# Kernel optimization log

Hardware: AMD Instinct MI355X
Metric: run time of the kernel (lower is better)

## Reference

```python
import jax, jax.numpy as jnp
import numpy as np

B, S, HIDDEN = 2, 2048, 1024
NUM_HEADS, HEAD_DIM = 16, 64
STRIDE = 128
NEG = -10000.0


def _strided_mask(seq_len):
    # Sparse Transformer strided pattern: causal, local window of STRIDE,
    # plus every STRIDE-th previous position.
    i = jnp.arange(seq_len)[:, None]
    j = jnp.arange(seq_len)[None, :]
    diff = i - j
    allowed = (diff >= 0) & ((diff < STRIDE) | (diff % STRIDE == 0))
    return jnp.where(allowed, 0.0, NEG).astype(jnp.float32)  # [S, S]


def setup_inputs() -> dict:
    key = jax.random.key(0)
    k0, k1, k2, k3, k4 = jax.random.split(key, 5)
    hidden_states = jax.random.normal(k0, (B, S, HIDDEN), dtype=jnp.float32)
    attention_mask = jnp.zeros((B, 1, 1, S), dtype=jnp.float32)
    W_q = jax.random.normal(k1, (HIDDEN, HIDDEN), dtype=jnp.float32) * 0.02
    b_q = jnp.zeros((HIDDEN,), dtype=jnp.float32)
    W_v = jax.random.normal(k2, (HIDDEN, HIDDEN), dtype=jnp.float32) * 0.02
    b_v = jnp.zeros((HIDDEN,), dtype=jnp.float32)
    return {"hidden_states": hidden_states, "attention_mask": attention_mask,
            "W_q": W_q, "b_q": b_q, "W_v": W_v, "b_v": b_v}


def _heads(x):
    b, s, _ = x.shape
    return x.reshape(b, s, NUM_HEADS, HEAD_DIM).transpose(0, 2, 1, 3)  # [B,H,S,d]


def reference(hidden_states, attention_mask, W_q, b_q, W_v, b_v):
    q = _heads(hidden_states @ W_q + b_q)  # [B,H,S,d]
    v = _heads(hidden_states @ W_v + b_v)  # [B,H,S,d]
    hash_mask = _strided_mask(q.shape[-2])  # [S,S], broadcast over B,H
    # NB: source computes matmul(query, query^T) -- Q used for both sides.
    scores = jnp.einsum('bhid,bhjd->bhij', q, q) + hash_mask
    scores = scores / jnp.sqrt(jnp.asarray(HEAD_DIM, scores.dtype))
    scores = scores + attention_mask
    probs = jax.nn.softmax(scores, axis=-1)  # dropout p=0 (eval)
    ctx = jnp.einsum('bhij,bhjd->bhid', probs, v)  # [B,H,S,d]
    b = ctx.shape[0]
    return ctx.transpose(0, 2, 1, 3).reshape(b, -1, NUM_HEADS * HEAD_DIM)
```

## Files before the change

kernel.cpp:

```cpp
#include <hip/hip_runtime.h>

typedef __attribute__((ext_vector_type(8))) short short8;
typedef __attribute__((ext_vector_type(4))) float float4v;

__device__ inline float bf2f(ushort u) {
    unsigned v = ((unsigned)u) << 16;
    return __builtin_bit_cast(float, v);
}
__device__ inline ushort f2bf(float f) {
    unsigned u = __builtin_bit_cast(unsigned, f);
    u += 0x7FFFu + ((u >> 16) & 1u);
    return (ushort)(u >> 16);
}

__global__ __launch_bounds__(256) void transpose_w(
    const float* __restrict__ Wq, const float* __restrict__ Wv,
    ushort* __restrict__ Wtq, ushort* __restrict__ Wtv) {
    __shared__ ushort tile[64][68];
    const float* W = blockIdx.z ? Wv : Wq;
    ushort* Wt     = blockIdx.z ? Wtv : Wtq;
    const int k0 = blockIdx.y * 64, n0 = blockIdx.x * 64;
    const int tid = threadIdx.x;
    const int rr = tid >> 4;
    const int cc = (tid & 15) * 4;
    union U4 { ushort u[4]; uint2 v; };
#pragma unroll
    for (int i = 0; i < 4; ++i) {
        int row = rr + i * 16;
        float4v f = *(const float4v*)(W + (size_t)(k0 + row) * 1024 + n0 + cc);
        U4 x;
#pragma unroll
        for (int j = 0; j < 4; ++j) x.u[j] = f2bf(f[j]);
        *(uint2*)&tile[row][cc] = x.v;
    }
    __syncthreads();
#pragma unroll
    for (int i = 0; i < 4; ++i) {
        int row = rr + i * 16;
        U4 o;
#pragma unroll
        for (int j = 0; j < 4; ++j) o.u[j] = tile[cc + j][row];
        *(uint2*)(Wt + (size_t)(n0 + row) * 1024 + k0 + cc) = o.v;
    }
}

__global__ __launch_bounds__(256) void qv_gemm(
    const float* __restrict__ hs,
    const ushort* __restrict__ Wtq, const ushort* __restrict__ Wtv,
    const float* __restrict__ bq, const float* __restrict__ bv,
    ushort* __restrict__ q_ws, ushort* __restrict__ v_ws) {
    __shared__ ushort Al[128][72];
    __shared__ ushort Bl[128][72];
    const ushort* Wt  = blockIdx.z ? Wtv : Wtq;
    const float* bias = blockIdx.z ? bv : bq;
    ushort* out       = blockIdx.z ? v_ws : q_ws;
    const int m0 = blockIdx.y * 128;
    const int n0 = blockIdx.x * 128;
    const int tid = threadIdx.x;
    const int wid = tid >> 6, lane = tid & 63;
    const int quad = lane >> 4, l16 = lane & 15;
    const int wm = (wid >> 1) * 64, wn = (wid & 1) * 64;

    float4v acc[4][4] = {};

    for (int kt = 0; kt < 1024; kt += 64) {
        __syncthreads();
#pragma unroll
        for (int i = 0; i < 4; ++i) {
            int c = tid + i * 256;
            int row = c >> 3, col = (c & 7) * 8;
            const float* src = hs + (size_t)(m0 + row) * 1024 + kt + col;
            float4v f0 = *(const float4v*)(src);
            float4v f1 = *(const float4v*)(src + 4);
            union { ushort u[8]; uint4 v; } pk;
#pragma unroll
            for (int j = 0; j < 4; ++j) { pk.u[j] = f2bf(f0[j]); pk.u[4 + j] = f2bf(f1[j]); }
            *(uint4*)&Al[row][col] = pk.v;
            *(uint4*)&Bl[row][col] = *(const uint4*)(Wt + (size_t)(n0 + row) * 1024 + kt + col);
        }
        __syncthreads();
#pragma unroll
        for (int ks = 0; ks < 2; ++ks) {
            short8 af[4], bfr[4];
#pragma unroll
            for (int mt = 0; mt < 4; ++mt)
                af[mt] = *(const short8*)&Al[wm + mt * 16 + l16][ks * 32 + quad * 8];
#pragma unroll
            for (int nt = 0; nt < 4; ++nt)
                bfr[nt] = *(const short8*)&Bl[wn + nt * 16 + l16][ks * 32 + quad * 8];
#pragma unroll
            for (int mt = 0; mt < 4; ++mt)
#pragma unroll
                for (int nt = 0; nt < 4; ++nt)
                    acc[mt][nt] = __builtin_amdgcn_mfma_f32_16x16x32_bf16(
                        af[mt], bfr[nt], acc[mt][nt], 0, 0, 0);
        }
    }
#pragma unroll
    for (int mt = 0; mt < 4; ++mt) {
#pragma unroll
        for (int nt = 0; nt < 4; ++nt) {
            int coln = n0 + wn + nt * 16 + l16;
            float bsv = bias[coln];
            int hh = coln >> 6, dd = coln & 63;
#pragma unroll
            for (int reg = 0; reg < 4; ++reg) {
                int r = m0 + wm + mt * 16 + quad * 4 + reg;
                int bb = r >> 11, s = r & 2047;
                out[(((size_t)bb * 16 + hh) * 2048 + s) * 64 + dd] =
                    f2bf(acc[mt][nt][reg] + bsv);
            }
        }
    }
}

__global__ __launch_bounds__(512) void attn(
    const ushort* __restrict__ q_ws, const ushort* __restrict__ v_ws,
    const float* __restrict__ amask, float* __restrict__ out) {
    const int t = blockIdx.x, h = blockIdx.y, b = blockIdx.z;

    __shared__ ushort Kw[256][72];
    __shared__ ushort Vt[64][266];
    __shared__ ushort Pl[128][266];
    __shared__ float  Sstr[128][17];
    __shared__ float  am[2048];

    const int tid = threadIdx.x;
    const int wid = tid >> 6, lane = tid & 63;
    const int quad = lane >> 4, l16 = lane & 15;
    const int r0 = wid * 16;
    const size_t qbase = ((size_t)b * 16 + h) * 2048 * 64;
    const int base_row = (t - 1) * 128;
    const int nk = (t >= 2) ? (t - 1) : 0;

    *(float4v*)&am[tid * 4] = *(const float4v*)(amask + (size_t)b * 2048 + tid * 4);
#pragma unroll
    for (int i = 0; i < 4; ++i) {
        int c = tid + i * 512;
        int row = c >> 3, col = (c & 7) * 8;
        int jg = base_row + row; if (jg < 0) jg = 0;
        *(uint4*)&Kw[row][col] = *(const uint4*)(q_ws + qbase + (size_t)jg * 64 + col);
    }
    {
        int j = tid & 255, dh0 = (tid >> 8) * 32;
        int jg = base_row + j; if (jg < 0) jg = 0;
        const ushort* src = v_ws + qbase + (size_t)jg * 64 + dh0;
#pragma unroll
        for (int d = 0; d < 32; d += 8) {
            union { uint4 v; ushort u[8]; } tmp;
            tmp.v = *(const uint4*)(src + d);
#pragma unroll
            for (int jj = 0; jj < 8; ++jj) Vt[dh0 + d + jj][j] = tmp.u[jj];
        }
    }
    __syncthreads();

    float4v sacc[16] = {};
#pragma unroll
    for (int ks = 0; ks < 2; ++ks) {
        short8 af = *(const short8*)&Kw[128 + r0 + l16][ks * 32 + quad * 8];
#pragma unroll
        for (int nt = 0; nt < 16; ++nt) {
            short8 bfr = *(const short8*)&Kw[nt * 16 + l16][ks * 32 + quad * 8];
            sacc[nt] = __builtin_amdgcn_mfma_f32_16x16x32_bf16(af, bfr, sacc[nt], 0, 0, 0);
        }
    }

    const int sr = tid >> 2;
    const int dq = (tid & 3) * 16;
    if (nk > 0) {
        float qv[16];
#pragma unroll
        for (int d = 0; d < 16; d += 8) {
            union { uint4 v; ushort u[8]; } tmp;
            tmp.v = *(const uint4*)&Kw[128 + sr][dq + d];
#pragma unroll
            for (int j = 0; j < 8; ++j) qv[d + j] = bf2f(tmp.u[j]);
        }
        for (int k = 0; k < nk; ++k) {
            const ushort* kr = q_ws + qbase + (size_t)(k * 128 + sr) * 64 + dq;
            float p = 0.f;
#pragma unroll
            for (int d = 0; d < 16; d += 8) {
                union { uint4 v; ushort u[8]; } tmp;
                tmp.v = *(const uint4*)(kr + d);
#pragma unroll
                for (int jj = 0; jj < 8; ++jj) p += qv[d + jj] * bf2f(tmp.u[jj]);
            }
            p += __shfl_xor(p, 1);
            p += __shfl_xor(p, 2);
            if ((tid & 3) == 0)
                Sstr[sr][k] = p * 0.125f + am[k * 128 + sr];
        }
    }
    __syncthreads();

#pragma unroll
    for (int reg = 0; reg < 4; ++reg) {
        int rr = r0 + quad * 4 + reg;
        float sv[16];
#pragma unroll
        for (int nt = 0; nt < 16; ++nt) {
            int c = nt * 16 + l16;
            bool allowed = (c >= rr) && (c <= rr + 128) && (t > 0 || c >= 128);
            int ci = base_row + c; if (ci < 0) ci = 0;
            sv[nt] = allowed ? sacc[nt][reg] * 0.125f + am[ci] : -INFINITY;
        }
        float sstr_v = (l16 < nk) ? Sstr[rr][l16] : -INFINITY;
        float m = sstr_v;
#pragma unroll
        for (int nt = 0; nt < 16; ++nt) m = fmaxf(m, sv[nt]);
#pragma unroll
        for (int off = 1; off < 16; off <<= 1) m = fmaxf(m, __shfl_xor(m, off));

        float es = (l16 < nk) ? __expf(sstr_v - m) : 0.f;
        float sum = es;
#pragma unroll
        for (int nt = 0; nt < 16; ++nt) {
            float e = (sv[nt] == -INFINITY) ? 0.f : __expf(sv[nt] - m);
            sv[nt] = e; sum += e;
        }
#pragma unroll
        for (int off = 1; off < 16; off <<= 1) sum += __shfl_xor(sum, off);
        float rden = 1.f / sum;
#pragma unroll
        for (int nt = 0; nt < 16; ++nt)
            Pl[rr][nt * 16 + l16] = f2bf(sv[nt] * rden);
        if (l16 < nk)
            Sstr[rr][l16] = es * rden;
    }
    __syncthreads();

    float4v cacc[4] = {};
#pragma unroll
    for (int ks = 0; ks < 8; ++ks) {
        short8 af = *(const short8*)&Pl[r0 + l16][ks * 32 + quad * 8];
#pragma unroll
        for (int nt = 0; nt < 4; ++nt) {
            short8 bfr = *(const short8*)&Vt[nt * 16 + l16][ks * 32 + quad * 8];
            cacc[nt] = __builtin_amdgcn_mfma_f32_16x16x32_bf16(af, bfr, cacc[nt], 0, 0, 0);
        }
    }
    __syncthreads();

    float* ctxp = (float*)&Pl[0][0];
    {
        float acc16[16] = {};
        for (int k = 0; k < nk; ++k) {
            float p = Sstr[sr][k];
            const ushort* vr = v_ws + qbase + (size_t)(k * 128 + sr) * 64 + dq;
#pragma unroll
            for (int d = 0; d < 16; d += 8) {
                union { uint4 v; ushort u[8]; } tmp;
                tmp.v = *(const uint4*)(vr + d);
#pragma unroll
                for (int j = 0; j < 8; ++j) acc16[d + j] += p * bf2f(tmp.u[j]);
            }
        }
#pragma unroll
        for (int d = 0; d < 16; d += 4)
            *(float4v*)&ctxp[sr * 68 + dq + d] = *(const float4v*)&acc16[d];
    }
    __syncthreads();

    const size_t obase = ((size_t)b * 2048 + (size_t)t * 128) * 1024 + (size_t)h * 64;
#pragma unroll
    for (int nt = 0; nt < 4; ++nt)
#pragma unroll
        for (int reg = 0; reg < 4; ++reg) {
            int rr = r0 + quad * 4 + reg;
            int d = nt * 16 + l16;
            out[obase + (size_t)rr * 1024 + d] = cacc[nt][reg] + ctxp[rr * 68 + d];
        }
}

extern "C" void kernel_launch(void* const* d_in, const int* in_sizes, int n_in,
                              void* d_out, int out_size, void* d_ws, size_t ws_size,
                              hipStream_t stream) {
    int ihs = -1, iam = -1, iw1 = -1, iw2 = -1, ib1 = -1, ib2 = -1;
    for (int i = 0; i < n_in; ++i) {
        int s = in_sizes[i];
        if      (s == 4194304) { if (ihs < 0) ihs = i; }
        else if (s == 4096)    { if (iam < 0) iam = i; }
        else if (s == 1048576) { if (iw1 < 0) iw1 = i; else if (iw2 < 0) iw2 = i; }
        else if (s == 1024)    { if (ib1 < 0) ib1 = i; else if (ib2 < 0) ib2 = i; }
    }
    if (ihs < 0) ihs = 0; if (iam < 0) iam = 1;
    if (iw1 < 0) iw1 = 2; if (ib1 < 0) ib1 = 3;
    if (iw2 < 0) iw2 = 4; if (ib2 < 0) ib2 = 5;

    const float* hs    = (const float*)d_in[ihs];
    const float* amask = (const float*)d_in[iam];
    const float* Wq    = (const float*)d_in[iw1];
    const float* bq    = (const float*)d_in[ib1];
    const float* Wv    = (const float*)d_in[iw2];
    const float* bv    = (const float*)d_in[ib2];
    float* out = (float*)d_out;

    char* ws = (char*)d_ws;
    ushort* Wtq  = (ushort*)(ws);
    ushort* Wtv  = (ushort*)(ws + (1u << 21));
    ushort* q_ws = (ushort*)(ws + (2u << 21));
    ushort* v_ws = (ushort*)(ws + (2u << 21) + (1u << 23));

    transpose_w<<<dim3(16, 16, 2), 256, 0, stream>>>(Wq, Wv, Wtq, Wtv);
    qv_gemm<<<dim3(8, 32, 2), 256, 0, stream>>>(hs, Wtq, Wtv, bq, bv, q_ws, v_ws);
    attn<<<dim3(16, 16, 2), 512, 0, stream>>>(q_ws, v_ws, amask, out);
}
```

Baseline: 157.5 us.

## Pre-convert hidden states to bf16 and stage GEMM tiles via direct global-to-LDS loads

Adds a separate kernel that converts hidden_states to bf16 once, so the QV GEMM no longer converts fp32 to bf16 inside every tile load. The GEMM then fills its shared-memory tiles with global_load_lds direct copies into unpadded 64-wide rows. The attention grid is also remapped so that neighbouring blocks cover different heads with the same t. The costs are an extra launch plus a bf16 copy of the activations round-tripping through memory, and likely LDS bank conflicts now that row padding is gone.

```diff
diff --git a/kernel.cpp b/kernel.cpp
--- a/kernel.cpp
+++ b/kernel.cpp
@@ -11,6 +11,27 @@
     unsigned u = __builtin_bit_cast(unsigned, f);
     u += 0x7FFFu + ((u >> 16) & 1u);
     return (ushort)(u >> 16);
+}
+
+__device__ inline void gload_lds16(const ushort* g, ushort* l) {
+    __builtin_amdgcn_global_load_lds(
+        (const __attribute__((address_space(1))) unsigned int*)g,
+        (__attribute__((address_space(3))) unsigned int*)l,
+        16, 0, 0);
+}
+
+__global__ __launch_bounds__(256) void convert_hs(
+    const float* __restrict__ hs, ushort* __restrict__ hsb) {
+    const size_t base = ((size_t)blockIdx.x * 256 + threadIdx.x) * 16;
+    union { ushort u[16]; uint4 v[2]; } o;
+#pragma unroll
+    for (int q = 0; q < 4; ++q) {
+        float4v f = *(const float4v*)(hs + base + q * 4);
+#pragma unroll
+        for (int j = 0; j < 4; ++j) o.u[q * 4 + j] = f2bf(f[j]);
+    }
+    *(uint4*)(hsb + base)     = o.v[0];
+    *(uint4*)(hsb + base + 8) = o.v[1];
 }
 
 __global__ __launch_bounds__(256) void transpose_w(
@@ -45,38 +66,34 @@
 }
 
 __global__ __launch_bounds__(256) void qv_gemm(
-    const float* __restrict__ hs,
+    const ushort* __restrict__ hsb,
     const ushort* __restrict__ Wtq, const ushort* __restrict__ Wtv,
     const float* __restrict__ bq, const float* __restrict__ bv,
     ushort* __restrict__ q_ws, ushort* __restrict__ v_ws) {
-    __shared__ ushort Al[128][72];
-    __shared__ ushort Bl[128][72];
+    __shared__ ushort Al[128 * 64];
+    __shared__ ushort Bl[128 * 64];
     const ushort* Wt  = blockIdx.z ? Wtv : Wtq;
     const float* bias = blockIdx.z ? bv : bq;
     ushort* out       = blockIdx.z ? v_ws : q_ws;
-    const int m0 = blockIdx.y * 128;
-    const int n0 = blockIdx.x * 128;
+    const int m0 = blockIdx.y * 128, n0 = blockIdx.x * 128;
     const int tid = threadIdx.x;
     const int wid = tid >> 6, lane = tid & 63;
     const int quad = lane >> 4, l16 = lane & 15;
     const int wm = (wid >> 1) * 64, wn = (wid & 1) * 64;
+    const int rbase = 32 * wid;
+    const int srow = lane >> 3, scol = (lane & 7) * 8;
 
     float4v acc[4][4] = {};
 
     for (int kt = 0; kt < 1024; kt += 64) {
         __syncthreads();
 #pragma unroll
-        for (int i = 0; i < 4; ++i) {
-            int c = tid + i * 256;
-            int row = c >> 3, col = (c & 7) * 8;
-            const float* src = hs + (size_t)(m0 + row) * 1024 + kt + col;
-            float4v f0 = *(const float4v*)(src);
-            float4v f1 = *(const float4v*)(src + 4);
-            union { ushort u[8]; uint4 v; } pk;
-#pragma unroll
-            for (int j = 0; j < 4; ++j) { pk.u[j] = f2bf(f0[j]); pk.u[4 + j] = f2bf(f1[j]); }
-            *(uint4*)&Al[row][col] = pk.v;
-            *(uint4*)&Bl[row][col] = *(const uint4*)(Wt + (size_t)(n0 + row) * 1024 + kt + col);
+        for (int c8 = 0; c8 < 4; ++c8) {
+            int row = rbase + c8 * 8;
+            gload_lds16(hsb + (size_t)(m0 + row + srow) * 1024 + kt + scol,
+                        &Al[row * 64]);
+            gload_lds16(Wt + (size_t)(n0 + row + srow) * 1024 + kt + scol,
+                        &Bl[row * 64]);
         }
         __syncthreads();
 #pragma unroll
@@ -84,10 +101,10 @@
             short8 af[4], bfr[4];
 #pragma unroll
             for (int mt = 0; mt < 4; ++mt)
-                af[mt] = *(const short8*)&Al[wm + mt * 16 + l16][ks * 32 + quad * 8];
+                af[mt] = *(const short8*)&Al[(wm + mt * 16 + l16) * 64 + (ks * 4 + quad) * 8];
 #pragma unroll
             for (int nt = 0; nt < 4; ++nt)
-                bfr[nt] = *(const short8*)&Bl[wn + nt * 16 + l16][ks * 32 + quad * 8];
+                bfr[nt] = *(const short8*)&Bl[(wn + nt * 16 + l16) * 64 + (ks * 4 + quad) * 8];
 #pragma unroll
             for (int mt = 0; mt < 4; ++mt)
 #pragma unroll
@@ -117,7 +134,11 @@
 __global__ __launch_bounds__(512) void attn(
     const ushort* __restrict__ q_ws, const ushort* __restrict__ v_ws,
     const float* __restrict__ amask, float* __restrict__ out) {
-    const int t = blockIdx.x, h = blockIdx.y, b = blockIdx.z;
+    const int lin = blockIdx.x + 16 * blockIdx.y;
+    const int u8 = lin & 7, v32 = lin >> 3;
+    const int t = v32 & 15;
+    const int h = u8 + ((v32 >> 4) << 3);
+    const int b = blockIdx.z;
 
     __shared__ ushort Kw[256][72];
     __shared__ ushort Vt[64][266];
@@ -300,10 +321,12 @@
     char* ws = (char*)d_ws;
     ushort* Wtq  = (ushort*)(ws);
     ushort* Wtv  = (ushort*)(ws + (1u << 21));
-    ushort* q_ws = (ushort*)(ws + (2u << 21));
-    ushort* v_ws = (ushort*)(ws + (2u << 21) + (1u << 23));
-
+    ushort* hsb  = (ushort*)(ws + (2u << 21));
+    ushort* q_ws = (ushort*)(ws + (2u << 21) + (1u << 23));
+    ushort* v_ws = (ushort*)(ws + (2u << 21) + (2u << 23));
+
+    convert_hs<<<1024, 256, 0, stream>>>(hs, hsb);
     transpose_w<<<dim3(16, 16, 2), 256, 0, stream>>>(Wq, Wv, Wtq, Wtv);
-    qv_gemm<<<dim3(8, 32, 2), 256, 0, stream>>>(hs, Wtq, Wtv, bq, bv, q_ws, v_ws);
+    qv_gemm<<<dim3(8, 32, 2), 256, 0, stream>>>(hsb, Wtq, Wtv, bq, bv, q_ws, v_ws);
     attn<<<dim3(16, 16, 2), 512, 0, stream>>>(q_ws, v_ws, amask, out);
 }
```

Measured after the change: 152.1 us. 1.04x faster.
